# Optimization experiments

Hardware: AMD Instinct MI355X
Metric: run time of the kernel (lower is better)

Reference implementation:

```python
import jax, jax.numpy as jnp
import numpy as np

BATCH, SEQ, FEAT, NUM_BINS = 64, 1024, 512, 32


def setup_inputs() -> dict:
    key = jax.random.key(0)
    k1, k2 = jax.random.split(key)
    features = jax.random.normal(k1, (BATCH, SEQ, FEAT), dtype=jnp.float32)
    # buffer: randn(input_dim, num_bins) / sqrt(input_dim)
    random_projection = jax.random.normal(k2, (FEAT, NUM_BINS), dtype=jnp.float32) / np.sqrt(FEAT)
    return {"features": features, "random_projection": random_projection}


def reference(features, random_projection):
    batch, seq, feat = features.shape
    x = features.reshape(-1, feat)  # [N, feat]
    N = x.shape[0]

    # RunningMeanStd.update from fresh state (mean=0, var=1, count=1e-4)
    eps_count = 1e-4
    batch_mean = x.mean(axis=0)
    batch_var = jnp.var(x, axis=0, ddof=1)  # torch.var is unbiased by default
    tot = eps_count + N
    delta = batch_mean  # - 0
    mean = delta * N / tot
    M2 = 1.0 * eps_count + batch_var * N + (delta ** 2) * eps_count * N / tot
    var = M2 / tot
    sigma = jnp.sqrt(var + 1e-8)

    normalized = (x - mean) / sigma
    projected = normalized @ random_projection  # [N, num_bins]
    bits = (projected > 0).astype(jnp.int64)
    pow2 = jnp.left_shift(jnp.int64(1), jnp.arange(NUM_BINS, dtype=jnp.int64))
    keys = (bits * pow2).sum(axis=-1)  # [N], values < 2^32

    # env_indices=None path: env = arange(N) % batch
    env = jnp.arange(N, dtype=jnp.int64) % batch
    combined = jnp.left_shift(env, 32) | keys  # unique (env, key) id

    # running occurrence count of each (env, key) in sample order i=0..N-1
    order = jnp.argsort(combined, stable=True)  # stable: preserves sample order within group
    s = combined[order]
    idx = jnp.arange(N, dtype=jnp.int64)
    is_start = jnp.concatenate([jnp.ones((1,), bool), s[1:] != s[:-1]])
    seg_start = jax.lax.cummax(jnp.where(is_start, idx, 0))
    occ = idx - seg_start + 1  # 1-based occurrence within group
    counts = jnp.zeros((N,), jnp.int64).at[order].set(occ)

    rewards = 1.0 / jnp.sqrt(counts.astype(features.dtype))
    return rewards.reshape(batch, seq, 1)
```

## Files before the change

### kernel.cpp

```cpp
#include <hip/hip_runtime.h>

using u16 = unsigned short;
using u64 = unsigned long long;
typedef short s16x8 __attribute__((ext_vector_type(8)));
typedef _Float16 f16x8 __attribute__((ext_vector_type(8)));
typedef float f32x4 __attribute__((ext_vector_type(4)));

constexpr int BATCH = 64, SEQ = 1024, FEAT = 512, NBINS = 32;
constexpr int N = BATCH * SEQ;
constexpr int TAB = 131072;
constexpr unsigned TABMASK = TAB - 1;
constexpr u64 EMPTY = ~0ull;
constexpr double FXSCALE = 67108864.0;
constexpr int NSHADOW = 64;


constexpr size_t OFF_KEYS = 0;
constexpr size_t OFF_HEAD = 1048576;
constexpr size_t OFF_CNT = 1572864;
constexpr size_t OFF_SHAD = 2097152;
constexpr size_t OFF_QD = 2621504;
constexpr size_t OFF_CD = 2752576;
constexpr size_t OFF_CF = 2818304;
constexpr size_t OFF_SLOT = 2818432;
constexpr size_t OFF_NEXT = 3080576;
constexpr size_t OFF_QFRAG = 3342720;

__device__ inline u16 f2h(float f) {
  _Float16 h = (_Float16)f;
  return __builtin_bit_cast(u16, h);
}

__global__ __launch_bounds__(256, 4) void colstats_kernel(
    const float4* __restrict__ xv,
    u64* __restrict__ shad) {
  const int t = threadIdx.x;
  const int L = blockIdx.x * 256 + t;
  double s0 = 0, s1 = 0, s2 = 0, s3 = 0, q0 = 0, q1 = 0, q2 = 0, q3 = 0;
  for (int mm = 0; mm < 32; mm += 8) {
    float4 v[8];
#pragma unroll
    for (int u = 0; u < 8; u++) v[u] = xv[L + (mm + u) * 262144];
#pragma unroll
    for (int u = 0; u < 8; u++) {
      double a = (double)v[u].x, b = (double)v[u].y;
      double c = (double)v[u].z, d = (double)v[u].w;
      s0 += a; s1 += b; s2 += c; s3 += d;
      q0 += a * a; q1 += b * b; q2 += c * c; q3 += d * d;
    }
  }
  __shared__ double red[256 * 8];
  red[t * 8 + 0] = s0; red[t * 8 + 1] = s1; red[t * 8 + 2] = s2; red[t * 8 + 3] = s3;
  red[t * 8 + 4] = q0; red[t * 8 + 5] = q1; red[t * 8 + 6] = q2; red[t * 8 + 7] = q3;
  __syncthreads();
  if (t < 128) {
    double v[8];
#pragma unroll
    for (int u = 0; u < 8; u++) v[u] = red[t * 8 + u] + red[(t + 128) * 8 + u];
    const int c0 = 4 * t;
    u64* sh = shad + (size_t)(blockIdx.x & (NSHADOW - 1)) * 1024;
#pragma unroll
    for (int u = 0; u < 4; u++) {
      long long a = (long long)llrint(v[u] * FXSCALE);
      long long b = (long long)llrint(v[4 + u] * FXSCALE);
      atomicAdd(&sh[c0 + u], (u64)a);
      atomicAdd(&sh[512 + c0 + u], (u64)b);
    }
  }
}

__global__ __launch_bounds__(512) void finalize_kernel(
    const float* __restrict__ P,
    const u64* __restrict__ shad,
    double* __restrict__ Qd, u16* __restrict__ qfrag,
    double* __restrict__ cd, float* __restrict__ cf) {
  __shared__ double meanArr[FEAT];
  __shared__ double invArr[FEAT];
  __shared__ double part[16][NBINS];
  const int t = threadIdx.x;
  long long isum = 0, isumsq = 0;
  for (int sh = 0; sh < NSHADOW; sh++) {
    isum += (long long)shad[sh * 1024 + t];
    isumsq += (long long)shad[sh * 1024 + 512 + t];
  }
  const double Nd = (double)N;
  const double tot = 1e-4 + Nd;
  double s = (double)isum * (1.0 / FXSCALE);
  double ss = (double)isumsq * (1.0 / FXSCALE);
  double bm = s / Nd;
  double bv = (ss - s * s / Nd) / (Nd - 1.0);
  double mean = bm * Nd / tot;
  double M2 = 1e-4 + bv * Nd + bm * bm * 1e-4 * Nd / tot;
  double var = M2 / tot;
  double inv = 1.0 / sqrt(var + 1e-8);
  meanArr[t] = mean;
  invArr[t] = inv;
  const int ch = t >> 7, ks = (t >> 5) & 3, kg = (t >> 3) & 3, jlo = t & 7;
#pragma unroll
  for (int j = 0; j < NBINS; j++) {
    double qd = (double)P[t * NBINS + j] * inv;
    Qd[t * NBINS + j] = qd;
    const int lane = (j & 15) | (kg << 4);
    const int bt = j >> 4;
    qfrag[(size_t)((((ch * 4 + ks) * 2 + bt) * 64 + lane) * 8 + jlo)] =
        f2h((float)qd);
  }
  __syncthreads();
  {
    const int j = t & 31, g = t >> 5;
    double p = 0.0;
    for (int f = g * 32; f < g * 32 + 32; f++) {
      double qd = (double)P[f * NBINS + j] * invArr[f];
      p += meanArr[f] * qd;
    }
    part[g][j] = p;
  }
  __syncthreads();
  if (t < NBINS) {
    double c = 0.0;
    for (int g = 0; g < 16; g++) c += part[g][t];
    cd[t] = c;
    cf[t] = (float)c;
  }
}

constexpr float TAU = 4e-3f;
__global__ __launch_bounds__(256) void project_kernel(
    const float* __restrict__ feat,
    const u16* __restrict__ qfrag, const float* __restrict__ cf,
    const double* __restrict__ Qd, const double* __restrict__ cd,
    u64* __restrict__ keys_tab, int* __restrict__ head,
    unsigned* __restrict__ cnt, int* __restrict__ slot, int* __restrict__ nxt) {
  const int t = threadIdx.x;
  const int lane = t & 63;
  const int w = t >> 6;
  const int rowBase = blockIdx.x * 64;
  const int arow = rowBase + w * 16 + (lane & 15);
  const float* xbase = feat + (size_t)arow * FEAT + (lane >> 4) * 8;

  f32x4 acc0 = {0.f, 0.f, 0.f, 0.f};
  f32x4 acc1 = {0.f, 0.f, 0.f, 0.f};
  for (int ch = 0; ch < 4; ch++) {
    s16x8 B[4][2];
#pragma unroll
    for (int ks = 0; ks < 4; ks++)
#pragma unroll
      for (int bt = 0; bt < 2; bt++)
        B[ks][bt] = *(const s16x8*)&qfrag[(size_t)((((ch * 4 + ks) * 2 + bt) * 64 + lane) * 8)];
#pragma unroll
    for (int ks = 0; ks < 4; ks++) {
      float4 x0 = *(const float4*)(xbase + ch * 128 + ks * 32);
      float4 x1 = *(const float4*)(xbase + ch * 128 + ks * 32 + 4);
      f16x8 a;
      a[0] = (_Float16)x0.x; a[1] = (_Float16)x0.y;
      a[2] = (_Float16)x0.z; a[3] = (_Float16)x0.w;
      a[4] = (_Float16)x1.x; a[5] = (_Float16)x1.y;
      a[6] = (_Float16)x1.z; a[7] = (_Float16)x1.w;
      acc0 = __builtin_amdgcn_mfma_f32_16x16x32_f16(
          a, __builtin_bit_cast(f16x8, B[ks][0]), acc0, 0, 0, 0);
      acc1 = __builtin_amdgcn_mfma_f32_16x16x32_f16(
          a, __builtin_bit_cast(f16x8, B[ks][1]), acc1, 0, 0, 0);
    }
  }
  const int colbin = lane & 15;
  float m0[4], m1[4];
  bool b0[4], b1[4];
  const float c0v = cf[colbin], c1v = cf[16 + colbin];
#pragma unroll
  for (int rg = 0; rg < 4; rg++) {
    m0[rg] = acc0[rg] - c0v;
    m1[rg] = acc1[rg] - c1v;
    b0[rg] = m0[rg] > 0.0f;
    b1[rg] = m1[rg] > 0.0f;
  }
#pragma unroll
  for (int bt = 0; bt < 2; bt++)
#pragma unroll
    for (int rg = 0; rg < 4; rg++) {
      const float mv = (bt == 0) ? m0[rg] : m1[rg];
      u64 mask = __ballot(fabsf(mv) < TAU);
      while (mask) {
        const int L = (int)__builtin_ctzll(mask);
        mask &= mask - 1;
        const int jj = bt * 16 + (L & 15);
        const int row = rowBase + w * 16 + (L >> 4) * 4 + rg;
        const float* xr = feat + (size_t)row * FEAT + lane * 8;
        const double* qp = Qd + (size_t)(lane * 8) * NBINS + jj;
        double p = 0.0;
#pragma unroll
        for (int u = 0; u < 8; u++) p = fma((double)xr[u], qp[u * NBINS], p);
#pragma unroll
        for (int off = 32; off > 0; off >>= 1) p += __shfl_xor(p, off, 64);
        const bool bit = p > cd[jj];
        if (lane == L) {
          if (bt == 0) b0[rg] = bit; else b1[rg] = bit;
        }
      }
    }
  unsigned kb0 = (b0[0] ? (1u << colbin) : 0u) | (b1[0] ? (1u << (16 + colbin)) : 0u);
  unsigned kb1 = (b0[1] ? (1u << colbin) : 0u) | (b1[1] ? (1u << (16 + colbin)) : 0u);
  unsigned kb2 = (b0[2] ? (1u << colbin) : 0u) | (b1[2] ? (1u << (16 + colbin)) : 0u);
  unsigned kb3 = (b0[3] ? (1u << colbin) : 0u) | (b1[3] ? (1u << (16 + colbin)) : 0u);
#pragma unroll
  for (int off = 1; off < 16; off <<= 1) {
    kb0 |= __shfl_xor(kb0, off, 64);
    kb1 |= __shfl_xor(kb1, off, 64);
    kb2 |= __shfl_xor(kb2, off, 64);
    kb3 |= __shfl_xor(kb3, off, 64);
  }
  const int sub = lane & 15;
  if (sub < 4) {
    const unsigned key = sub == 0 ? kb0 : sub == 1 ? kb1 : sub == 2 ? kb2 : kb3;
    const int i = rowBase + w * 16 + (lane >> 4) * 4 + sub;
    const u64 combined = (u64)key;
    unsigned idx = (unsigned)((combined * 0x9E3779B97F4A7C15ull) >> 47) & TABMASK;
    for (;;) {
      u64 prev = atomicCAS(&keys_tab[idx], EMPTY, combined);
      if (prev == EMPTY || prev == combined) break;
      idx = (idx + 1) & TABMASK;
    }
    slot[i] = (int)idx;
    atomicAdd(&cnt[idx], 1u);
    nxt[i] = atomicExch(&head[idx], i);
  }
}

__global__ __launch_bounds__(256) void count_kernel(
    const int* __restrict__ slot, const int* __restrict__ nxt,
    const int* __restrict__ head, const unsigned* __restrict__ cnt,
    float* __restrict__ out) {
  const int i = blockIdx.x * 256 + threadIdx.x;
  const int sl = slot[i];
  const unsigned c = cnt[sl];
  float r = 1.0f;
  if (c > 1u) {
    int j = head[sl];
    int occ = 1;
    while (j >= 0) {
      occ += (j < i) ? 1 : 0;
      j = nxt[j];
    }
    r = 1.0f / sqrtf((float)occ);
  }
  out[i] = r;
}

extern "C" void kernel_launch(void* const* d_in, const int* in_sizes, int n_in,
                              void* d_out, int out_size, void* d_ws, size_t ws_size,
                              hipStream_t stream) {
  const float4* xv = (const float4*)d_in[0];
  const float* feat = (const float*)d_in[0];
  const float* proj = (const float*)d_in[1];
  float* out = (float*)d_out;
  char* ws = (char*)d_ws;

  u64* keys_tab = (u64*)(ws + OFF_KEYS);
  int* head = (int*)(ws + OFF_HEAD);
  unsigned* cnt = (unsigned*)(ws + OFF_CNT);
  u64* shad = (u64*)(ws + OFF_SHAD);
  double* Qd = (double*)(ws + OFF_QD);
  double* cd = (double*)(ws + OFF_CD);
  float* cf = (float*)(ws + OFF_CF);
  int* slot = (int*)(ws + OFF_SLOT);
  int* nxt = (int*)(ws + OFF_NEXT);
  u16* qfrag = (u16*)(ws + OFF_QFRAG);

  (void)hipMemsetAsync(ws + OFF_KEYS, 0xFF, OFF_CNT - OFF_KEYS, stream);
  (void)hipMemsetAsync(ws + OFF_CNT, 0x00, OFF_QD - OFF_CNT, stream);

  colstats_kernel<<<1024, 256, 0, stream>>>(xv, shad);
  finalize_kernel<<<1, 512, 0, stream>>>(proj, shad, Qd, qfrag, cd, cf);
  project_kernel<<<N / 64, 256, 0, stream>>>(feat, qfrag, cf, Qd, cd,
                                             keys_tab, head, cnt, slot, nxt);
  count_kernel<<<N / 256, 256, 0, stream>>>(slot, nxt, head, cnt, out);
}
```

Measured before the change: 272.0 us.

## Replace shadow atomics with per-block partials, fold memsets into colstats kernel

Column-statistics blocks now write their fixed-point sums to per-block partial slots instead of atomically adding into 64 shadow copies. A small merge kernel reduces those partials and atomically adds them into a single merged array, so the single-block finalize kernel reads one value per column instead of looping over shadows. The two workspace memsets are removed, and the hash-table and counter initialisation is done by the colstats threads instead. Blocks grow to 512 threads with a 4-way shared-memory reduction. The cost is one extra kernel launch and a few MB more workspace traffic.

```diff
diff --git a/kernel.cpp b/kernel.cpp
--- a/kernel.cpp
+++ b/kernel.cpp
@@ -12,30 +12,39 @@
 constexpr unsigned TABMASK = TAB - 1;
 constexpr u64 EMPTY = ~0ull;
 constexpr double FXSCALE = 67108864.0;
-constexpr int NSHADOW = 64;
+constexpr int NBLK_A = 512;
 
 
 constexpr size_t OFF_KEYS = 0;
 constexpr size_t OFF_HEAD = 1048576;
 constexpr size_t OFF_CNT = 1572864;
-constexpr size_t OFF_SHAD = 2097152;
-constexpr size_t OFF_QD = 2621504;
-constexpr size_t OFF_CD = 2752576;
-constexpr size_t OFF_CF = 2818304;
-constexpr size_t OFF_SLOT = 2818432;
-constexpr size_t OFF_NEXT = 3080576;
-constexpr size_t OFF_QFRAG = 3342720;
+constexpr size_t OFF_MERGE = 2097152;
+constexpr size_t OFF_PART = 2105344;
+constexpr size_t OFF_QD = 6299648;
+constexpr size_t OFF_CD = 6430720;
+constexpr size_t OFF_CF = 6430976;
+constexpr size_t OFF_SLOT = 6431104;
+constexpr size_t OFF_NEXT = 6693248;
+constexpr size_t OFF_QFRAG = 6955392;
+
+constexpr int INIT_FF_U4 = 1572864 / 16;
+constexpr int INIT_TOT_U4 = 2105344 / 16;
 
 __device__ inline u16 f2h(float f) {
   _Float16 h = (_Float16)f;
   return __builtin_bit_cast(u16, h);
 }
 
-__global__ __launch_bounds__(256, 4) void colstats_kernel(
+__global__ __launch_bounds__(512, 4) void colstats_kernel(
     const float4* __restrict__ xv,
-    u64* __restrict__ shad) {
+    uint4* __restrict__ ws4,
+    long long* __restrict__ part) {
   const int t = threadIdx.x;
-  const int L = blockIdx.x * 256 + t;
+  const int L = blockIdx.x * 512 + t;
+  if (L < INIT_TOT_U4) {
+    const unsigned v = (L < INIT_FF_U4) ? 0xFFFFFFFFu : 0u;
+    ws4[L] = make_uint4(v, v, v, v);
+  }
   double s0 = 0, s1 = 0, s2 = 0, s3 = 0, q0 = 0, q1 = 0, q2 = 0, q3 = 0;
   for (int mm = 0; mm < 32; mm += 8) {
     float4 v[8];
@@ -49,40 +58,47 @@
       q0 += a * a; q1 += b * b; q2 += c * c; q3 += d * d;
     }
   }
-  __shared__ double red[256 * 8];
+  __shared__ double red[512 * 8];
   red[t * 8 + 0] = s0; red[t * 8 + 1] = s1; red[t * 8 + 2] = s2; red[t * 8 + 3] = s3;
   red[t * 8 + 4] = q0; red[t * 8 + 5] = q1; red[t * 8 + 6] = q2; red[t * 8 + 7] = q3;
   __syncthreads();
   if (t < 128) {
     double v[8];
 #pragma unroll
-    for (int u = 0; u < 8; u++) v[u] = red[t * 8 + u] + red[(t + 128) * 8 + u];
+    for (int u = 0; u < 8; u++)
+      v[u] = ((red[t * 8 + u] + red[(t + 128) * 8 + u]) +
+              red[(t + 256) * 8 + u]) + red[(t + 384) * 8 + u];
     const int c0 = 4 * t;
-    u64* sh = shad + (size_t)(blockIdx.x & (NSHADOW - 1)) * 1024;
+    long long* pp = part + (size_t)blockIdx.x * 1024;
 #pragma unroll
     for (int u = 0; u < 4; u++) {
-      long long a = (long long)llrint(v[u] * FXSCALE);
-      long long b = (long long)llrint(v[4 + u] * FXSCALE);
-      atomicAdd(&sh[c0 + u], (u64)a);
-      atomicAdd(&sh[512 + c0 + u], (u64)b);
-    }
-  }
+      pp[c0 + u] = (long long)llrint(v[u] * FXSCALE);
+      pp[512 + c0 + u] = (long long)llrint(v[4 + u] * FXSCALE);
+    }
+  }
+}
+
+__global__ __launch_bounds__(256) void merge_kernel(
+    const long long* __restrict__ part, u64* __restrict__ merged) {
+  const int T = blockIdx.x * 256 + threadIdx.x;
+  const int c = T & 1023, g = T >> 10;
+  long long s = 0;
+#pragma unroll 8
+  for (int b = g * 32; b < g * 32 + 32; b++) s += part[(size_t)b * 1024 + c];
+  atomicAdd(&merged[c], (u64)s);
 }
 
 __global__ __launch_bounds__(512) void finalize_kernel(
     const float* __restrict__ P,
-    const u64* __restrict__ shad,
+    const u64* __restrict__ merged,
     double* __restrict__ Qd, u16* __restrict__ qfrag,
     double* __restrict__ cd, float* __restrict__ cf) {
   __shared__ double meanArr[FEAT];
   __shared__ double invArr[FEAT];
   __shared__ double part[16][NBINS];
   const int t = threadIdx.x;
-  long long isum = 0, isumsq = 0;
-  for (int sh = 0; sh < NSHADOW; sh++) {
-    isum += (long long)shad[sh * 1024 + t];
-    isumsq += (long long)shad[sh * 1024 + 512 + t];
-  }
+  const long long isum = (long long)merged[t];
+  const long long isumsq = (long long)merged[512 + t];
   const double Nd = (double)N;
   const double tot = 1e-4 + Nd;
   double s = (double)isum * (1.0 / FXSCALE);
@@ -257,7 +273,8 @@
   u64* keys_tab = (u64*)(ws + OFF_KEYS);
   int* head = (int*)(ws + OFF_HEAD);
   unsigned* cnt = (unsigned*)(ws + OFF_CNT);
-  u64* shad = (u64*)(ws + OFF_SHAD);
+  u64* merged = (u64*)(ws + OFF_MERGE);
+  long long* part = (long long*)(ws + OFF_PART);
   double* Qd = (double*)(ws + OFF_QD);
   double* cd = (double*)(ws + OFF_CD);
   float* cf = (float*)(ws + OFF_CF);
@@ -265,11 +282,9 @@
   int* nxt = (int*)(ws + OFF_NEXT);
   u16* qfrag = (u16*)(ws + OFF_QFRAG);
 
-  (void)hipMemsetAsync(ws + OFF_KEYS, 0xFF, OFF_CNT - OFF_KEYS, stream);
-  (void)hipMemsetAsync(ws + OFF_CNT, 0x00, OFF_QD - OFF_CNT, stream);
-
-  colstats_kernel<<<1024, 256, 0, stream>>>(xv, shad);
-  finalize_kernel<<<1, 512, 0, stream>>>(proj, shad, Qd, qfrag, cd, cf);
+  colstats_kernel<<<NBLK_A, 512, 0, stream>>>(xv, (uint4*)ws, part);
+  merge_kernel<<<64, 256, 0, stream>>>(part, merged);
+  finalize_kernel<<<1, 512, 0, stream>>>(proj, merged, Qd, qfrag, cd, cf);
   project_kernel<<<N / 64, 256, 0, stream>>>(feat, qfrag, cf, Qd, cd,
                                              keys_tab, head, cnt, slot, nxt);
   count_kernel<<<N / 256, 256, 0, stream>>>(slot, nxt, head, cnt, out);
```

Measured after the change: 253.4 us. 1.07x faster.
